# Kernel tuning notes

Hardware: AMD Instinct MI355X
Metric: run time of the kernel (lower is better)

Reference implementation:

```python
import jax, jax.numpy as jnp
import numpy as np

D = 768; H = 6; HD = D // H; DFF = 2048
L = 512; S = 1024; B = 8
EPS = 1e-5
SCALE = 1.0 / float(np.sqrt(2 * D // H))  # fused q/k head_dim = 2*D/H (Conditional-DETR attention)


def _ln(x, g, b):
    m = x.mean(-1, keepdims=True)
    v = ((x - m) ** 2).mean(-1, keepdims=True)
    return (x - m) / jnp.sqrt(v + EPS) * g + b


def _lin(x, w, b):  # w: (out, in) torch convention
    return jnp.einsum('lbd,ed->lbe', x, w) + b


def _fuse(c, p):  # channel-concat per head: (L,B,D)x2 -> (L,B,H,2*HD)
    Lx, Bx, _ = c.shape
    c = c.reshape(Lx, Bx, H, HD)
    p = p.reshape(Lx, Bx, H, HD)
    return jnp.concatenate([c, p], axis=-1)


def _attn(q, k, v, ow, ob):
    # q:(L,B,H,2HD) k:(S,B,H,2HD) v:(S,B,D); out_proj maps vdim->vdim
    Lx, Bx = q.shape[0], q.shape[1]
    Sx = k.shape[0]
    vh = v.reshape(Sx, Bx, H, HD)
    scores = jnp.einsum('lbhd,sbhd->bhls', q * SCALE, k)
    w = jax.nn.softmax(scores, axis=-1)
    o = jnp.einsum('bhls,sbhe->lbhe', w, vh).reshape(Lx, Bx, D)
    return _lin(o, ow, ob), w.mean(axis=1)  # head-averaged attn weights (B,L,S)


def setup_inputs() -> dict:
    key = jax.random.key(0)
    ks = iter(jax.random.split(key, 64))
    d = {}
    d['tgt'] = jax.random.normal(next(ks), (L, B, D), jnp.float32)
    d['memory'] = jax.random.normal(next(ks), (S, B, D), jnp.float32)
    d['tgt_pos'] = jax.random.normal(next(ks), (L, B, D), jnp.float32)
    d['memory_pos'] = jax.random.normal(next(ks), (S, B, D), jnp.float32)
    d['tgt_pos2'] = jax.random.normal(next(ks), (L, B, D), jnp.float32)

    def W(shape):
        return jax.random.normal(next(ks), shape, jnp.float32) * 0.02

    for pre in ('sa', 'ca'):
        for nm in ('qc', 'qp', 'kc', 'kp', 'v', 'o'):
            d[f'{pre}_{nm}_w'] = W((D, D))
            d[f'{pre}_{nm}_b'] = jnp.zeros((D,), jnp.float32)
    d['ff1_w'] = W((DFF, D)); d['ff1_b'] = jnp.zeros((DFF,), jnp.float32)
    d['ff2_w'] = W((D, DFF)); d['ff2_b'] = jnp.zeros((D,), jnp.float32)
    for i in (1, 2, 3):
        d[f'ln{i}_g'] = jnp.ones((D,), jnp.float32)
        d[f'ln{i}_b'] = jnp.zeros((D,), jnp.float32)
    return d


def reference(tgt, memory, tgt_pos, memory_pos, tgt_pos2,
              sa_qc_w, sa_qc_b, sa_qp_w, sa_qp_b, sa_kc_w, sa_kc_b, sa_kp_w, sa_kp_b,
              sa_v_w, sa_v_b, sa_o_w, sa_o_b,
              ca_qc_w, ca_qc_b, ca_qp_w, ca_qp_b, ca_kc_w, ca_kc_b, ca_kp_w, ca_kp_b,
              ca_v_w, ca_v_b, ca_o_w, ca_o_b,
              ff1_w, ff1_b, ff2_w, ff2_b,
              ln1_g, ln1_b, ln2_g, ln2_b, ln3_g, ln3_b):
    # --- self attention (dropout = identity at inference) ---
    q = _fuse(_lin(tgt_pos, sa_qc_w, sa_qc_b), _lin(tgt, sa_qp_w, sa_qp_b))
    k = _fuse(_lin(tgt_pos, sa_kc_w, sa_kc_b), _lin(tgt, sa_kp_w, sa_kp_b))
    v = _lin(tgt, sa_v_w, sa_v_b)
    t2, self_att = _attn(q, k, v, sa_o_w, sa_o_b)
    t = _ln(tgt + t2, ln1_g, ln1_b)
    # --- cross attention ---
    q = _fuse(_lin(tgt_pos, ca_qc_w, ca_qc_b), _lin(t + tgt_pos2, ca_qp_w, ca_qp_b))
    k = _fuse(_lin(memory, ca_kc_w, ca_kc_b), _lin(memory_pos, ca_kp_w, ca_kp_b))
    v = _lin(memory_pos, ca_v_w, ca_v_b)
    t2, att = _attn(q, k, v, ca_o_w, ca_o_b)
    t = _ln(t + t2, ln2_g, ln2_b)
    # --- FFN + post-norm ---
    t2 = _lin(jax.nn.relu(_lin(t, ff1_w, ff1_b)), ff2_w, ff2_b)
    t = _ln(t + t2, ln3_g, ln3_b)
    return (t, att, self_att)
```

## Files before the change

### kernel.cpp

```cpp
#include <hip/hip_runtime.h>


typedef __bf16 bf16;
typedef __attribute__((ext_vector_type(8))) __bf16 bf16x8;
typedef __attribute__((ext_vector_type(4))) float f32x4;

#define D_MODEL 768
#define NH 6
#define HD 128
#define ROWSTRIDE (8 * D_MODEL)

__device__ inline void swz_xyz(int& x, int& y, int& z) {
    const int nx = gridDim.x, ny = gridDim.y;
    const int n = nx * ny * gridDim.z;
    const int flat = blockIdx.x + nx * (blockIdx.y + ny * blockIdx.z);
    const int t = (flat & 7) * (n >> 3) + (flat >> 3);
    x = t % nx;
    const int r = t / nx;
    y = r % ny;
    z = r / ny;
}

__device__ __forceinline__ void gld16(const bf16* g, bf16* l) {
    __builtin_amdgcn_global_load_lds(
        (const __attribute__((address_space(1))) unsigned int*)g,
        (__attribute__((address_space(3))) unsigned int*)l, 16, 0, 0);
}

__device__ inline bf16x8 ld8f(const float* p) {
    f32x4 a = *(const f32x4*)p, b = *(const f32x4*)(p + 4);
    bf16x8 r;
#pragma unroll
    for (int i = 0; i < 4; i++) { r[i] = (bf16)a[i]; r[i + 4] = (bf16)b[i]; }
    return r;
}
__device__ inline bf16x8 ld8bf(const bf16* p, const float* q) {
    bf16x8 x = *(const bf16x8*)p;
    f32x4 a = *(const f32x4*)q, b = *(const f32x4*)(q + 4);
    bf16x8 r;
#pragma unroll
    for (int i = 0; i < 4; i++) { r[i] = (bf16)((float)x[i] + a[i]); r[i + 4] = (bf16)((float)x[i + 4] + b[i]); }
    return r;
}
__device__ inline bf16x8 ld8ff(const float* p, const float* q) {
    f32x4 a = *(const f32x4*)p, b = *(const f32x4*)(p + 4);
    f32x4 c = *(const f32x4*)q, d = *(const f32x4*)(q + 4);
    bf16x8 r;
#pragma unroll
    for (int i = 0; i < 4; i++) { r[i] = (bf16)(a[i] + c[i]); r[i + 4] = (bf16)(b[i] + d[i]); }
    return r;
}

struct CvtJob { const float* src; const float* src2; const bf16* add; bf16* dst; int nvec; };
struct CvtJobs { CvtJob j[12]; };

__global__ __launch_bounds__(256) void cvt_multi(CvtJobs jobs)
{
    const CvtJob jb = jobs.j[blockIdx.y];
    const int stride = gridDim.x * 256;
    if (jb.src2) {
        for (int i = blockIdx.x * 256 + threadIdx.x; i < jb.nvec; i += stride)
            *(bf16x8*)(jb.dst + (size_t)i * 8) = ld8ff(jb.src + (size_t)i * 8, jb.src2 + (size_t)i * 8);
    } else if (jb.add) {
        for (int i = blockIdx.x * 256 + threadIdx.x; i < jb.nvec; i += stride)
            *(bf16x8*)(jb.dst + (size_t)i * 8) = ld8bf(jb.add + (size_t)i * 8, jb.src + (size_t)i * 8);
    } else {
        for (int i = blockIdx.x * 256 + threadIdx.x; i < jb.nvec; i += stride)
            *(bf16x8*)(jb.dst + (size_t)i * 8) = ld8f(jb.src + (size_t)i * 8);
    }
}

struct JobB { const bf16* A; const bf16* W; const float* bias; bf16* C; int relu; };
struct JobsB { JobB j[5]; };

__global__ __launch_bounds__(256) void gemm_bb(
    JobsB jobs, int lda, int ldw, int ldc, int K)
{
    __shared__ __align__(16) bf16 As[2][128 * 32];
    __shared__ __align__(16) bf16 Bs[2][128 * 32];
    int bx, by, bz;
    swz_xyz(bx, by, bz);
    const JobB jb = jobs.j[bz];
    const int bm = by * 128, bn = bx * 128;
    const int tid = threadIdx.x;
    const int wave = tid >> 6, lane = tid & 63;
    const int wm = (wave >> 1) * 64, wn = (wave & 1) * 64;
    const int quad = lane >> 4, m16 = lane & 15;
    const int crow = lane >> 2, ccol = (lane & 3) * 8;
    const bf16* a0 = jb.A + (size_t)(bm + wave * 32 + crow) * lda + ccol;
    const bf16* a1 = a0 + (size_t)16 * lda;
    const bf16* w0 = jb.W + (size_t)(bn + wave * 32 + crow) * ldw + ccol;
    const bf16* w1 = w0 + (size_t)16 * ldw;
    const int wo = wave * 1024;
    f32x4 acc[4][4] = {};
    gld16(a0, As[0] + wo);
    gld16(a1, As[0] + wo + 512);
    gld16(w0, Bs[0] + wo);
    gld16(w1, Bs[0] + wo + 512);
    __syncthreads();
    int cur = 0;
    for (int k0 = 0; k0 < K; k0 += 32) {
        const int kn = k0 + 32;
        if (kn < K) {
            bf16* dA = As[cur ^ 1] + wo;
            bf16* dB = Bs[cur ^ 1] + wo;
            gld16(a0 + kn, dA);
            gld16(a1 + kn, dA + 512);
            gld16(w0 + kn, dB);
            gld16(w1 + kn, dB + 512);
        }
        const bf16* rA = As[cur];
        const bf16* rB = Bs[cur];
        bf16x8 af[4], bfr[4];
#pragma unroll
        for (int i = 0; i < 4; i++) {
            af[i]  = *(const bf16x8*)&rA[(wm + i * 16 + m16) * 32 + quad * 8];
            bfr[i] = *(const bf16x8*)&rB[(wn + i * 16 + m16) * 32 + quad * 8];
        }
#pragma unroll
        for (int i = 0; i < 4; i++)
#pragma unroll
            for (int j = 0; j < 4; j++)
                acc[i][j] = __builtin_amdgcn_mfma_f32_16x16x32_bf16(af[i], bfr[j], acc[i][j], 0, 0, 0);
        __syncthreads();
        cur ^= 1;
    }
#pragma unroll
    for (int j = 0; j < 4; j++) {
        const int col = bn + wn + j * 16 + m16;
        const float bv = jb.bias[col];
#pragma unroll
        for (int i = 0; i < 4; i++)
#pragma unroll
            for (int r = 0; r < 4; r++) {
                const int row = bm + wm + i * 16 + quad * 4 + r;
                float val = acc[i][j][r] + bv;
                if (jb.relu) val = fmaxf(val, 0.f);
                jb.C[(size_t)row * ldc + col] = (bf16)val;
            }
    }
}

__global__ __launch_bounds__(256) void gemm_sk_bb(
    const bf16* __restrict__ A, int lda, const bf16* __restrict__ W, int ldw,
    float* __restrict__ Cp, size_t cstride, int ldc, int Ks)
{
    __shared__ __align__(16) bf16 As[2][128 * 32];
    __shared__ __align__(16) bf16 Bs[2][128 * 32];
    int bx, by, bz;
    swz_xyz(bx, by, bz);
    const int bm = by * 128, bn = bx * 128;
    const int kbase = bz * Ks;
    const int tid = threadIdx.x;
    const int wave = tid >> 6, lane = tid & 63;
    const int wm = (wave >> 1) * 64, wn = (wave & 1) * 64;
    const int quad = lane >> 4, m16 = lane & 15;
    const int crow = lane >> 2, ccol = (lane & 3) * 8;
    const bf16* a0 = A + (size_t)(bm + wave * 32 + crow) * lda + kbase + ccol;
    const bf16* a1 = a0 + (size_t)16 * lda;
    const bf16* w0 = W + (size_t)(bn + wave * 32 + crow) * ldw + kbase + ccol;
    const bf16* w1 = w0 + (size_t)16 * ldw;
    const int wo = wave * 1024;
    f32x4 acc[4][4] = {};
    gld16(a0, As[0] + wo);
    gld16(a1, As[0] + wo + 512);
    gld16(w0, Bs[0] + wo);
    gld16(w1, Bs[0] + wo + 512);
    __syncthreads();
    int cur = 0;
    for (int k0 = 0; k0 < Ks; k0 += 32) {
        const int kn = k0 + 32;
        if (kn < Ks) {
            bf16* dA = As[cur ^ 1] + wo;
            bf16* dB = Bs[cur ^ 1] + wo;
            gld16(a0 + kn, dA);
            gld16(a1 + kn, dA + 512);
            gld16(w0 + kn, dB);
            gld16(w1 + kn, dB + 512);
        }
        const bf16* rA = As[cur];
        const bf16* rB = Bs[cur];
        bf16x8 af[4], bfr[4];
#pragma unroll
        for (int i = 0; i < 4; i++) {
            af[i]  = *(const bf16x8*)&rA[(wm + i * 16 + m16) * 32 + quad * 8];
            bfr[i] = *(const bf16x8*)&rB[(wn + i * 16 + m16) * 32 + quad * 8];
        }
#pragma unroll
        for (int i = 0; i < 4; i++)
#pragma unroll
            for (int j = 0; j < 4; j++)
                acc[i][j] = __builtin_amdgcn_mfma_f32_16x16x32_bf16(af[i], bfr[j], acc[i][j], 0, 0, 0);
        __syncthreads();
        cur ^= 1;
    }
    float* out = Cp + (size_t)bz * cstride;
#pragma unroll
    for (int j = 0; j < 4; j++) {
        const int col = bn + wn + j * 16 + m16;
#pragma unroll
        for (int i = 0; i < 4; i++)
#pragma unroll
            for (int r = 0; r < 4; r++) {
                const int row = bm + wm + i * 16 + quad * 4 + r;
                out[(size_t)row * ldc + col] = acc[i][j][r];
            }
    }
}

__global__ __launch_bounds__(256) void attn_scores(
    const bf16* __restrict__ qc, const bf16* __restrict__ qp,
    const bf16* __restrict__ kc, const bf16* __restrict__ kp,
    bf16* __restrict__ scores, int Lq, int S, float scale)
{
    __shared__ __align__(16) bf16 As[2][128 * 32];
    __shared__ __align__(16) bf16 Bs[2][128 * 32];
    int bx, by, bz;
    swz_xyz(bx, by, bz);
    const int bh = bz;
    const int b = bh / NH, h = bh % NH;
    const int bm = by * 128, bn = bx * 128;
    const int tid = threadIdx.x;
    const int wave = tid >> 6, lane = tid & 63;
    const int wm = (wave >> 1) * 64, wn = (wave & 1) * 64;
    const int quad = lane >> 4, m16 = lane & 15;
    const int crow = lane >> 2, ccol = (lane & 3) * 8;
    const size_t hb = (size_t)b * D_MODEL + h * HD;
    const size_t ar0 = (size_t)(bm + wave * 32 + crow) * ROWSTRIDE + hb + ccol;
    const size_t ar1 = ar0 + (size_t)16 * ROWSTRIDE;
    const size_t br0 = (size_t)(bn + wave * 32 + crow) * ROWSTRIDE + hb + ccol;
    const size_t br1 = br0 + (size_t)16 * ROWSTRIDE;
    const int wo = wave * 1024;
    f32x4 acc[4][4] = {};
    gld16(qc + ar0, As[0] + wo);
    gld16(qc + ar1, As[0] + wo + 512);
    gld16(kc + br0, Bs[0] + wo);
    gld16(kc + br1, Bs[0] + wo + 512);
    __syncthreads();
    int cur = 0;
    for (int k0 = 0; k0 < 256; k0 += 32) {
        const int kn = k0 + 32;
        if (kn < 256) {
            const bf16* qsrc = (kn < 128) ? qc : qp;
            const bf16* ksrc = (kn < 128) ? kc : kp;
            const int kcol = kn & 127;
            bf16* dA = As[cur ^ 1] + wo;
            bf16* dB = Bs[cur ^ 1] + wo;
            gld16(qsrc + ar0 + kcol, dA);
            gld16(qsrc + ar1 + kcol, dA + 512);
            gld16(ksrc + br0 + kcol, dB);
            gld16(ksrc + br1 + kcol, dB + 512);
        }
        const bf16* rA = As[cur];
        const bf16* rB = Bs[cur];
        bf16x8 af[4], bfr[4];
#pragma unroll
        for (int i = 0; i < 4; i++) {
            af[i]  = *(const bf16x8*)&rA[(wm + i * 16 + m16) * 32 + quad * 8];
            bfr[i] = *(const bf16x8*)&rB[(wn + i * 16 + m16) * 32 + quad * 8];
        }
#pragma unroll
        for (int i = 0; i < 4; i++)
#pragma unroll
            for (int j = 0; j < 4; j++)
                acc[i][j] = __builtin_amdgcn_mfma_f32_16x16x32_bf16(af[i], bfr[j], acc[i][j], 0, 0, 0);
        __syncthreads();
        cur ^= 1;
    }
    bf16* sb = scores + (size_t)bh * Lq * S;
#pragma unroll
    for (int i = 0; i < 4; i++)
#pragma unroll
        for (int j = 0; j < 4; j++)
#pragma unroll
            for (int r = 0; r < 4; r++)
                sb[(size_t)(bm + wm + i * 16 + quad * 4 + r) * S + bn + wn + j * 16 + m16]
                    = (bf16)(acc[i][j][r] * scale);
}

template <int N>
__global__ __launch_bounds__(256) void softmax_mean(
    bf16* __restrict__ scores, float* __restrict__ att, int Lq)
{
    const int S = N << 8;
    const int l = blockIdx.x, b = blockIdx.y;
    const int tid = threadIdx.x;
    __shared__ float red[4], red2[4];
    float macc[N];
#pragma unroll
    for (int i = 0; i < N; i++) macc[i] = 0.f;
    for (int h = 0; h < NH; h++) {
        bf16* p = scores + ((size_t)(b * NH + h) * Lq + l) * S;
        float vals[N];
        float mx = -1e30f;
#pragma unroll
        for (int i = 0; i < N; i++) { vals[i] = (float)p[tid + (i << 8)]; mx = fmaxf(mx, vals[i]); }
        for (int off = 32; off; off >>= 1) mx = fmaxf(mx, __shfl_xor(mx, off, 64));
        if ((tid & 63) == 0) red[tid >> 6] = mx;
        __syncthreads();
        mx = fmaxf(fmaxf(red[0], red[1]), fmaxf(red[2], red[3]));
        float sum = 0.f;
#pragma unroll
        for (int i = 0; i < N; i++) { vals[i] = __expf(vals[i] - mx); sum += vals[i]; }
        for (int off = 32; off; off >>= 1) sum += __shfl_xor(sum, off, 64);
        if ((tid & 63) == 0) red2[tid >> 6] = sum;
        __syncthreads();
        const float inv = 1.f / (red2[0] + red2[1] + red2[2] + red2[3]);
#pragma unroll
        for (int i = 0; i < N; i++) {
            const float w = vals[i] * inv;
            p[tid + (i << 8)] = (bf16)w;
            macc[i] += w;
        }
    }
    float* ao = att + ((size_t)b * Lq + l) * S;
#pragma unroll
    for (int i = 0; i < N; i++) ao[tid + (i << 8)] = macc[i] * (1.f / 6.f);
}

__global__ __launch_bounds__(256) void attn_pv_sk(
    const bf16* __restrict__ wsm, const bf16* __restrict__ v,
    float* __restrict__ Pv, size_t pstride, int Lq, int S)
{
    __shared__ __align__(16) bf16 As[128 * 32];
    __shared__ __align__(16) bf16 BsT[128][40];
    int bx, by, bz;
    swz_xyz(bx, by, bz);
    const int bh = bz;
    const int b = bh / NH, h = bh % NH;
    const int bm = bx * 128;
    const int kbase = by * (S >> 1);
    const int tid = threadIdx.x;
    const int wave = tid >> 6, lane = tid & 63;
    const int wm = (wave >> 1) * 64, wn = (wave & 1) * 64;
    const int quad = lane >> 4, m16 = lane & 15;
    const int crow = lane >> 2, ccol = (lane & 3) * 8;
    const int kk0 = tid >> 4, e0 = (tid & 15) * 8;
    f32x4 acc[4][4] = {};
    const bf16* wbase = wsm + (size_t)(bh * Lq + bm) * S + kbase;
    const size_t vb = (size_t)b * D_MODEL + h * HD;
    const bf16* a0 = wbase + (size_t)(wave * 32 + crow) * S + ccol;
    const bf16* a1 = a0 + (size_t)16 * S;
    bf16* lA = As + wave * 1024;
    bf16x8 v0, v1;
    v0 = *(const bf16x8*)(v + (size_t)(kbase + kk0) * ROWSTRIDE + vb + e0);
    v1 = *(const bf16x8*)(v + (size_t)(kbase + kk0 + 16) * ROWSTRIDE + vb + e0);
    for (int k0 = 0; k0 < (S >> 1); k0 += 32) {
        gld16(a0 + k0, lA);
        gld16(a1 + k0, lA + 512);
#pragma unroll
        for (int i = 0; i < 8; i++) { BsT[e0 + i][kk0] = v0[i]; BsT[e0 + i][kk0 + 16] = v1[i]; }
        __syncthreads();
        const int kn = k0 + 32;
        if (kn < (S >> 1)) {
            v0 = *(const bf16x8*)(v + (size_t)(kbase + kn + kk0) * ROWSTRIDE + vb + e0);
            v1 = *(const bf16x8*)(v + (size_t)(kbase + kn + kk0 + 16) * ROWSTRIDE + vb + e0);
        }
        bf16x8 af[4], bfr[4];
#pragma unroll
        for (int i = 0; i < 4; i++) {
            af[i]  = *(const bf16x8*)&As[(wm + i * 16 + m16) * 32 + quad * 8];
            bfr[i] = *(const bf16x8*)&BsT[wn + i * 16 + m16][quad * 8];
        }
#pragma unroll
        for (int i = 0; i < 4; i++)
#pragma unroll
            for (int j = 0; j < 4; j++)
                acc[i][j] = __builtin_amdgcn_mfma_f32_16x16x32_bf16(af[i], bfr[j], acc[i][j], 0, 0, 0);
        __syncthreads();
    }
    float* out = Pv + by * pstride;
#pragma unroll
    for (int i = 0; i < 4; i++)
#pragma unroll
        for (int j = 0; j < 4; j++)
#pragma unroll
            for (int r = 0; r < 4; r++)
                out[(size_t)(bm + wm + i * 16 + quad * 4 + r) * ROWSTRIDE + vb + wn + j * 16 + m16]
                    = acc[i][j][r];
}

template <int NP, typename TR, typename TO>
__global__ __launch_bounds__(256) void add_ln_p(
    const TR* __restrict__ resid, const float* __restrict__ P, size_t pstride,
    const float* __restrict__ xbias,
    const float* __restrict__ g, const float* __restrict__ be, TO* __restrict__ out)
{
    const size_t base = (size_t)blockIdx.x * D_MODEL;
    const int tid = threadIdx.x;
    float v[3];
#pragma unroll
    for (int i = 0; i < 3; i++) {
        const int c = tid + (i << 8);
        float x = xbias[c];
#pragma unroll
        for (int p = 0; p < NP; p++) x += P[p * pstride + base + c];
        v[i] = (float)resid[base + c] + x;
    }
    float s = v[0] + v[1] + v[2];
    float s2 = v[0] * v[0] + v[1] * v[1] + v[2] * v[2];
    for (int off = 32; off; off >>= 1) { s += __shfl_xor(s, off, 64); s2 += __shfl_xor(s2, off, 64); }
    __shared__ float rs[4], rs2[4];
    if ((tid & 63) == 0) { rs[tid >> 6] = s; rs2[tid >> 6] = s2; }
    __syncthreads();
    s = rs[0] + rs[1] + rs[2] + rs[3];
    s2 = rs2[0] + rs2[1] + rs2[2] + rs2[3];
    const float mean = s * (1.f / 768.f);
    const float var = s2 * (1.f / 768.f) - mean * mean;
    const float inv = rsqrtf(var + 1e-5f);
#pragma unroll
    for (int i = 0; i < 3; i++) {
        const int c = tid + (i << 8);
        out[base + c] = (TO)((v[i] - mean) * inv * g[c] + be[c]);
    }
}

extern "C" void kernel_launch(void* const* d_in, const int* in_sizes, int n_in,
                              void* d_out, int out_size, void* d_ws, size_t ws_size,
                              hipStream_t stream)
{
    const float* tgt        = (const float*)d_in[0];
    const float* memory     = (const float*)d_in[1];
    const float* tgt_pos    = (const float*)d_in[2];
    const float* memory_pos = (const float*)d_in[3];
    const float* tgt_pos2   = (const float*)d_in[4];
    const float *sa_w[6], *sa_b[6], *ca_w[6], *ca_b[6];
    for (int i = 0; i < 6; i++) {
        sa_w[i] = (const float*)d_in[5 + 2 * i];  sa_b[i] = (const float*)d_in[6 + 2 * i];
        ca_w[i] = (const float*)d_in[17 + 2 * i]; ca_b[i] = (const float*)d_in[18 + 2 * i];
    }
    const float* ff1_w = (const float*)d_in[29]; const float* ff1_b = (const float*)d_in[30];
    const float* ff2_w = (const float*)d_in[31]; const float* ff2_b = (const float*)d_in[32];
    const float* ln_g[3] = {(const float*)d_in[33], (const float*)d_in[35], (const float*)d_in[37]};
    const float* ln_b[3] = {(const float*)d_in[34], (const float*)d_in[36], (const float*)d_in[38]};

    char* ws = (char*)d_ws;
    bf16* qc  = (bf16*)(ws);
    bf16* qp  = (bf16*)(ws + 6291456);
    bf16* kc  = (bf16*)(ws + 12582912);
    bf16* kp  = (bf16*)(ws + 25165824);
    bf16* vv  = (bf16*)(ws + 37748736);
    bf16* t1  = (bf16*)(ws + 50331648);
    bf16* sc  = (bf16*)(ws + 56623104);
    const size_t PSTRIDE = 3145728;
    float* pv_sa = (float*)(ws + 81788928);
    float* pv_ca = (float*)(ws + 12582912);
    float* op    = (float*)(ws + 56623104);
    float* fp    = (float*)(ws + 56623104);
    bf16*  tca   = kc;
    bf16*  ffh   = kp;

    bf16* tgt_b    = sc;
    bf16* mem_b    = sc;
    bf16* mempos_b = sc + 6291456;
    bf16* wb       = (bf16*)d_out;
    const size_t WSTEP = 589824;
    bf16* tp_b   = (bf16*)((char*)d_out + 12582912);
    bf16* qpin_b = tp_b + 3145728;
    bf16* ff1b   = qc;
    bf16* ff2b   = qp;
    bf16* savA   = kc;
    bf16* saw5b  = kc + 3145728;
    bf16* cavA   = vv;
    bf16* caw5b  = vv + 3145728;

    float* out_t    = (float*)d_out;
    float* out_att  = out_t + 3145728;
    float* out_satt = out_att + 4194304;

    const dim3 blk(256);
    const float SCALE = 0.0625f;

    {
        CvtJobs C = {};
        for (int i = 0; i < 5; i++) C.j[i] = {sa_w[i], nullptr, nullptr, wb + i * WSTEP, 73728};
        for (int i = 0; i < 3; i++) C.j[5 + i] = {ca_w[2 + i], nullptr, nullptr, wb + (5 + i) * WSTEP, 73728};
        C.j[8]  = {ca_w[0], nullptr, nullptr, wb + 8 * WSTEP, 73728};
        C.j[9]  = {ca_w[1], nullptr, nullptr, wb + 9 * WSTEP, 73728};
        C.j[10] = {tgt,     nullptr, nullptr, tgt_b, 393216};
        C.j[11] = {tgt_pos, nullptr, nullptr, tp_b,  393216};
        cvt_multi<<<dim3(288, 12), blk, 0, stream>>>(C);
    }

    {
        JobsB J = {};
        J.j[0] = {tp_b,  wb + 0 * WSTEP, sa_b[0], qc, 0};
        J.j[1] = {tgt_b, wb + 1 * WSTEP, sa_b[1], qp, 0};
        J.j[2] = {tp_b,  wb + 2 * WSTEP, sa_b[2], kc, 0};
        J.j[3] = {tgt_b, wb + 3 * WSTEP, sa_b[3], kp, 0};
        J.j[4] = {tgt_b, wb + 4 * WSTEP, sa_b[4], vv, 0};
        gemm_bb<<<dim3(6, 32, 5), blk, 0, stream>>>(J, 768, 768, 768, 768);
    }
    attn_scores<<<dim3(4, 4, 48), blk, 0, stream>>>(qc, qp, kc, kp, sc, 512, 512, SCALE);
    softmax_mean<2><<<dim3(512, 8), blk, 0, stream>>>(sc, out_satt, 512);
    attn_pv_sk<<<dim3(4, 2, 48), blk, 0, stream>>>(sc, vv, pv_sa, PSTRIDE, 512, 512);
    {
        CvtJobs C = {};
        C.j[0] = {pv_sa, pv_sa + PSTRIDE, nullptr, savA,  393216};
        C.j[1] = {sa_w[5], nullptr,       nullptr, saw5b, 73728};
        cvt_multi<<<dim3(288, 2), blk, 0, stream>>>(C);
    }
    gemm_sk_bb<<<dim3(6, 32, 2), blk, 0, stream>>>(savA, 768, saw5b, 768,
                                                   op, PSTRIDE, 768, 384);
    add_ln_p<2, float, bf16><<<dim3(4096), blk, 0, stream>>>(tgt, op, PSTRIDE, sa_b[5],
                                                             ln_g[0], ln_b[0], t1);

    {
        CvtJobs C = {};
        C.j[0] = {memory,     nullptr, nullptr, mem_b,    786432};
        C.j[1] = {memory_pos, nullptr, nullptr, mempos_b, 786432};
        C.j[2] = {tgt_pos2,   nullptr, t1,      qpin_b,   393216};
        cvt_multi<<<dim3(288, 3), blk, 0, stream>>>(C);
    }

    {
        JobsB J = {};
        J.j[0] = {tp_b,   wb + 8 * WSTEP, ca_b[0], qc, 0};
        J.j[1] = {qpin_b, wb + 9 * WSTEP, ca_b[1], qp, 0};
        gemm_bb<<<dim3(6, 32, 2), blk, 0, stream>>>(J, 768, 768, 768, 768);
    }
    {
        JobsB J = {};
        J.j[0] = {mem_b,    wb + 5 * WSTEP, ca_b[2], kc, 0};
        J.j[1] = {mempos_b, wb + 6 * WSTEP, ca_b[3], kp, 0};
        J.j[2] = {mempos_b, wb + 7 * WSTEP, ca_b[4], vv, 0};
        gemm_bb<<<dim3(6, 64, 3), blk, 0, stream>>>(J, 768, 768, 768, 768);
    }
    attn_scores<<<dim3(8, 4, 48), blk, 0, stream>>>(qc, qp, kc, kp, sc, 512, 1024, SCALE);
    {
        CvtJobs C = {};
        C.j[0] = {ff1_w, nullptr, nullptr, ff1b, 196608};
        C.j[1] = {ff2_w, nullptr, nullptr, ff2b, 196608};
        cvt_multi<<<dim3(288, 2), blk, 0, stream>>>(C);
    }
    softmax_mean<4><<<dim3(512, 8), blk, 0, stream>>>(sc, out_att, 512);
    attn_pv_sk<<<dim3(4, 2, 48), blk, 0, stream>>>(sc, vv, pv_ca, PSTRIDE, 512, 1024);
    {
        CvtJobs C = {};
        C.j[0] = {pv_ca, pv_ca + PSTRIDE, nullptr, cavA,  393216};
        C.j[1] = {ca_w[5], nullptr,       nullptr, caw5b, 73728};
        cvt_multi<<<dim3(288, 2), blk, 0, stream>>>(C);
    }
    gemm_sk_bb<<<dim3(6, 32, 2), blk, 0, stream>>>(cavA, 768, caw5b, 768,
                                                   op, PSTRIDE, 768, 384);
    add_ln_p<2, bf16, bf16><<<dim3(4096), blk, 0, stream>>>(t1, op, PSTRIDE, ca_b[5],
                                                            ln_g[1], ln_b[1], tca);

    {
        JobsB J = {};
        J.j[0] = {tca, ff1b, ff1_b, ffh, 1};
        gemm_bb<<<dim3(16, 32, 1), blk, 0, stream>>>(J, 768, 768, 2048, 768);
    }
    gemm_sk_bb<<<dim3(6, 32, 4), blk, 0, stream>>>(ffh, 2048, ff2b, 2048,
                                                   fp, PSTRIDE, 768, 512);
    add_ln_p<4, bf16, float><<<dim3(4096), blk, 0, stream>>>(tca, fp, PSTRIDE, ff2_b,
                                                             ln_g[2], ln_b[2], out_t);
}
```

Measured before the change: 613.3 us.

## Keep two K-tiles of global-to-LDS loads in flight in GEMM and score kernels

Restructures the main loop of the batched GEMM, split-K GEMM and attention-score kernels. Two stages are prefetched up front, and each iteration waits with an explicit vmcnt(4) so the next tile's loads stay outstanding while the current tile is computed. The freed buffer is refilled two tiles ahead, behind a pair of s_barriers. This hides more global-load latency than the previous single-ahead prefetch. The cost is hand-written waitcnt and barrier logic that the compiler can no longer reorder, plus an extra barrier per iteration.

```diff
diff --git a/kernel.cpp b/kernel.cpp
--- a/kernel.cpp
+++ b/kernel.cpp
@@ -9,6 +9,8 @@
 #define NH 6
 #define HD 128
 #define ROWSTRIDE (8 * D_MODEL)
+
+#define FENCE() asm volatile("" ::: "memory")
 
 __device__ inline void swz_xyz(int& x, int& y, int& z) {
     const int nx = gridDim.x, ny = gridDim.y;
@@ -93,24 +95,17 @@
     const bf16* w1 = w0 + (size_t)16 * ldw;
     const int wo = wave * 1024;
     f32x4 acc[4][4] = {};
-    gld16(a0, As[0] + wo);
-    gld16(a1, As[0] + wo + 512);
-    gld16(w0, Bs[0] + wo);
-    gld16(w1, Bs[0] + wo + 512);
-    __syncthreads();
-    int cur = 0;
-    for (int k0 = 0; k0 < K; k0 += 32) {
-        const int kn = k0 + 32;
-        if (kn < K) {
-            bf16* dA = As[cur ^ 1] + wo;
-            bf16* dB = Bs[cur ^ 1] + wo;
-            gld16(a0 + kn, dA);
-            gld16(a1 + kn, dA + 512);
-            gld16(w0 + kn, dB);
-            gld16(w1 + kn, dB + 512);
-        }
-        const bf16* rA = As[cur];
-        const bf16* rB = Bs[cur];
+    auto stage = [&](int buf, int k) {
+        bf16* dA = As[buf] + wo;
+        bf16* dB = Bs[buf] + wo;
+        gld16(a0 + k, dA);
+        gld16(a1 + k, dA + 512);
+        gld16(w0 + k, dB);
+        gld16(w1 + k, dB + 512);
+    };
+    auto compute = [&](int buf) {
+        const bf16* rA = As[buf];
+        const bf16* rB = Bs[buf];
         bf16x8 af[4], bfr[4];
 #pragma unroll
         for (int i = 0; i < 4; i++) {
@@ -122,9 +117,26 @@
 #pragma unroll
             for (int j = 0; j < 4; j++)
                 acc[i][j] = __builtin_amdgcn_mfma_f32_16x16x32_bf16(af[i], bfr[j], acc[i][j], 0, 0, 0);
-        __syncthreads();
+    };
+    stage(0, 0);
+    stage(1, 32);
+    int cur = 0;
+    for (int k0 = 0; k0 < K - 32; k0 += 32) {
+        asm volatile("s_waitcnt vmcnt(4)" ::: "memory");
+        __builtin_amdgcn_s_barrier();
+        FENCE();
+        compute(cur);
+        FENCE();
+        __builtin_amdgcn_s_barrier();
+        FENCE();
+        const int kp2 = k0 + 64;
+        if (kp2 < K) stage(cur, kp2);
         cur ^= 1;
     }
+    asm volatile("s_waitcnt vmcnt(0)" ::: "memory");
+    __builtin_amdgcn_s_barrier();
+    FENCE();
+    compute(cur);
 #pragma unroll
     for (int j = 0; j < 4; j++) {
         const int col = bn + wn + j * 16 + m16;
@@ -162,24 +174,17 @@
     const bf16* w1 = w0 + (size_t)16 * ldw;
     const int wo = wave * 1024;
     f32x4 acc[4][4] = {};
-    gld16(a0, As[0] + wo);
-    gld16(a1, As[0] + wo + 512);
-    gld16(w0, Bs[0] + wo);
-    gld16(w1, Bs[0] + wo + 512);
-    __syncthreads();
-    int cur = 0;
-    for (int k0 = 0; k0 < Ks; k0 += 32) {
-        const int kn = k0 + 32;
-        if (kn < Ks) {
-            bf16* dA = As[cur ^ 1] + wo;
-            bf16* dB = Bs[cur ^ 1] + wo;
-            gld16(a0 + kn, dA);
-            gld16(a1 + kn, dA + 512);
-            gld16(w0 + kn, dB);
-            gld16(w1 + kn, dB + 512);
-        }
-        const bf16* rA = As[cur];
-        const bf16* rB = Bs[cur];
+    auto stage = [&](int buf, int k) {
+        bf16* dA = As[buf] + wo;
+        bf16* dB = Bs[buf] + wo;
+        gld16(a0 + k, dA);
+        gld16(a1 + k, dA + 512);
+        gld16(w0 + k, dB);
+        gld16(w1 + k, dB + 512);
+    };
+    auto compute = [&](int buf) {
+        const bf16* rA = As[buf];
+        const bf16* rB = Bs[buf];
         bf16x8 af[4], bfr[4];
 #pragma unroll
         for (int i = 0; i < 4; i++) {
@@ -191,9 +196,26 @@
 #pragma unroll
             for (int j = 0; j < 4; j++)
                 acc[i][j] = __builtin_amdgcn_mfma_f32_16x16x32_bf16(af[i], bfr[j], acc[i][j], 0, 0, 0);
-        __syncthreads();
+    };
+    stage(0, 0);
+    stage(1, 32);
+    int cur = 0;
+    for (int k0 = 0; k0 < Ks - 32; k0 += 32) {
+        asm volatile("s_waitcnt vmcnt(4)" ::: "memory");
+        __builtin_amdgcn_s_barrier();
+        FENCE();
+        compute(cur);
+        FENCE();
+        __builtin_amdgcn_s_barrier();
+        FENCE();
+        const int kp2 = k0 + 64;
+        if (kp2 < Ks) stage(cur, kp2);
         cur ^= 1;
     }
+    asm volatile("s_waitcnt vmcnt(0)" ::: "memory");
+    __builtin_amdgcn_s_barrier();
+    FENCE();
+    compute(cur);
     float* out = Cp + (size_t)bz * cstride;
 #pragma unroll
     for (int j = 0; j < 4; j++) {
@@ -232,27 +254,20 @@
     const size_t br1 = br0 + (size_t)16 * ROWSTRIDE;
     const int wo = wave * 1024;
     f32x4 acc[4][4] = {};
-    gld16(qc + ar0, As[0] + wo);
-    gld16(qc + ar1, As[0] + wo + 512);
-    gld16(kc + br0, Bs[0] + wo);
-    gld16(kc + br1, Bs[0] + wo + 512);
-    __syncthreads();
-    int cur = 0;
-    for (int k0 = 0; k0 < 256; k0 += 32) {
-        const int kn = k0 + 32;
-        if (kn < 256) {
-            const bf16* qsrc = (kn < 128) ? qc : qp;
-            const bf16* ksrc = (kn < 128) ? kc : kp;
-            const int kcol = kn & 127;
-            bf16* dA = As[cur ^ 1] + wo;
-            bf16* dB = Bs[cur ^ 1] + wo;
-            gld16(qsrc + ar0 + kcol, dA);
-            gld16(qsrc + ar1 + kcol, dA + 512);
-            gld16(ksrc + br0 + kcol, dB);
-            gld16(ksrc + br1 + kcol, dB + 512);
-        }
-        const bf16* rA = As[cur];
-        const bf16* rB = Bs[cur];
+    auto stage = [&](int buf, int k) {
+        const bf16* qsrc = (k < 128) ? qc : qp;
+        const bf16* ksrc = (k < 128) ? kc : kp;
+        const int kcol = k & 127;
+        bf16* dA = As[buf] + wo;
+        bf16* dB = Bs[buf] + wo;
+        gld16(qsrc + ar0 + kcol, dA);
+        gld16(qsrc + ar1 + kcol, dA + 512);
+        gld16(ksrc + br0 + kcol, dB);
+        gld16(ksrc + br1 + kcol, dB + 512);
+    };
+    auto compute = [&](int buf) {
+        const bf16* rA = As[buf];
+        const bf16* rB = Bs[buf];
         bf16x8 af[4], bfr[4];
 #pragma unroll
         for (int i = 0; i < 4; i++) {
@@ -264,9 +279,26 @@
 #pragma unroll
             for (int j = 0; j < 4; j++)
                 acc[i][j] = __builtin_amdgcn_mfma_f32_16x16x32_bf16(af[i], bfr[j], acc[i][j], 0, 0, 0);
-        __syncthreads();
+    };
+    stage(0, 0);
+    stage(1, 32);
+    int cur = 0;
+    for (int k0 = 0; k0 < 224; k0 += 32) {
+        asm volatile("s_waitcnt vmcnt(4)" ::: "memory");
+        __builtin_amdgcn_s_barrier();
+        FENCE();
+        compute(cur);
+        FENCE();
+        __builtin_amdgcn_s_barrier();
+        FENCE();
+        const int kp2 = k0 + 64;
+        if (kp2 < 256) stage(cur, kp2);
         cur ^= 1;
     }
+    asm volatile("s_waitcnt vmcnt(0)" ::: "memory");
+    __builtin_amdgcn_s_barrier();
+    FENCE();
+    compute(cur);
     bf16* sb = scores + (size_t)bh * Lq * S;
 #pragma unroll
     for (int i = 0; i < 4; i++)
```

New measurement: 614.0 us. Within noise of the previous version (+0.1%).
